# Optimization experiments

Measured on AMD Instinct MI355X. Metric: run time of the kernel, lower is better.

The kernel has to match this reference:

```python
import jax, jax.numpy as jnp
import numpy as np

N = 25000
E = 400000
H = 4        # heads
C = 256      # per-head channels
D_IN = 1024
NEG_SLOPE = 0.2


def setup_inputs() -> dict:
    key = jax.random.key(0)
    k1, k2, k3, k4, k5, k6 = jax.random.split(key, 6)
    x = jax.random.normal(k1, (N, D_IN), dtype=jnp.float32)
    edge_index = jax.random.randint(k2, (2, E), 0, N, dtype=jnp.int64)
    # GATConv parameters
    scale = 1.0 / np.sqrt(D_IN)
    W = jax.random.normal(k3, (D_IN, H * C), dtype=jnp.float32) * scale
    att_src = jax.random.normal(k4, (H, C), dtype=jnp.float32) * 0.1
    att_dst = jax.random.normal(k5, (H, C), dtype=jnp.float32) * 0.1
    bias = jax.random.normal(k6, (H * C,), dtype=jnp.float32) * 0.01
    return {"x": x, "edge_index": edge_index, "W": W,
            "att_src": att_src, "att_dst": att_dst, "bias": bias}


def reference(x, edge_index, W, att_src, att_dst, bias):
    # Dense projection: [N, D_IN] @ [D_IN, H*C] -> [N, H, C]
    xp = (x @ W).reshape(N, H, C)

    # Per-node attention logits [N, H]
    a_src = jnp.einsum('nhc,hc->nh', xp, att_src)
    a_dst = jnp.einsum('nhc,hc->nh', xp, att_dst)

    # PyG default add_self_loops=True
    loops = jnp.arange(N, dtype=edge_index.dtype)
    src = jnp.concatenate([edge_index[0], loops])  # [E+N]
    dst = jnp.concatenate([edge_index[1], loops])  # [E+N]

    # Edge attention logits + LeakyReLU
    e = jax.nn.leaky_relu(a_src[src] + a_dst[dst], NEG_SLOPE)  # [E+N, H]

    # Segment softmax over destination nodes (every node has a self loop)
    m = jax.ops.segment_max(e, dst, num_segments=N)            # [N, H]
    ee = jnp.exp(e - m[dst])
    z = jax.ops.segment_sum(ee, dst, num_segments=N)           # [N, H]
    alpha = ee / z[dst]                                        # [E+N, H]

    # Scatter-weighted aggregation: out[i] = sum_j alpha_ij * xp[j]
    msgs = xp[src] * alpha[:, :, None]                         # [E+N, H, C]
    out = jax.ops.segment_sum(msgs, dst, num_segments=N)       # [N, H, C]

    out = out.reshape(N, H * C) + bias
    # dropout(0.5) is identity in eval mode; act = ReLU
    return jax.nn.relu(out)
```

## Files before the change

### kernel.cpp

```cpp
#include <hip/hip_runtime.h>
#include <hip/hip_bf16.h>
#include <stdint.h>

#define N_NODES 25000
#define M_PAD   25088
#define E_EDGES 400000
#define NE      (E_EDGES + N_NODES)
#define HEADS   4
#define D_DIM   1024
#define NEG_SLOPE 0.2f
#define NBLK_SCAN ((N_NODES + 255) / 256)

using bf16x8  = __attribute__((ext_vector_type(8))) short;
using floatx4 = __attribute__((ext_vector_type(4))) float;
using ushort8 = __attribute__((ext_vector_type(8))) unsigned short;

__device__ __forceinline__ unsigned short f2bf(float f) {
    union { float f; unsigned u; } v{f};
    unsigned r = v.u + 0x7fffu + ((v.u >> 16) & 1u);
    return (unsigned short)(r >> 16);
}
__device__ __forceinline__ float bf2f(unsigned short s) {
    union { unsigned u; float f; } v{(unsigned)s << 16};
    return v.f;
}

__global__ __launch_bounds__(256) void k_convert_x(
        const float* __restrict__ x, unsigned short* __restrict__ xb) {
    int i = blockIdx.x * 256 + threadIdx.x;
    int row = i >> 8;
    if (row >= M_PAD) return;
    ushort4 o;
    if (row < N_NODES) {
        float4 v = ((const float4*)x)[i];
        o = make_ushort4(f2bf(v.x), f2bf(v.y), f2bf(v.z), f2bf(v.w));
    } else {
        o = make_ushort4(0, 0, 0, 0);
    }
    ((ushort4*)xb)[i] = o;
}

__global__ void k_convert_wt(const float* __restrict__ W,
                             unsigned short* __restrict__ Wt) {
    __shared__ float tile[32][33];
    int bx = blockIdx.x, by = blockIdx.y;
    int tx = threadIdx.x, ty = threadIdx.y;
    #pragma unroll
    for (int i = 0; i < 32; i += 8) {
        int k = by * 32 + ty + i;
        int n = bx * 32 + tx;
        tile[ty + i][tx] = W[(size_t)k * D_DIM + n];
    }
    __syncthreads();
    #pragma unroll
    for (int i = 0; i < 32; i += 8) {
        int n = bx * 32 + ty + i;
        int k = by * 32 + tx;
        Wt[(size_t)n * D_DIM + k] = f2bf(tile[tx][ty + i]);
    }
}

__global__ __launch_bounds__(256) void k_gemm(
        const unsigned short* __restrict__ A,
        const unsigned short* __restrict__ Bt,
        unsigned short* __restrict__ C) {
    __shared__ __align__(16) unsigned short As[128 * 32];
    __shared__ __align__(16) unsigned short Bs[128 * 32];

    const int tid  = threadIdx.x;
    const int m0   = blockIdx.x * 128;
    const int n0   = blockIdx.y * 128;
    const int wave = tid >> 6, lane = tid & 63;
    const int wm   = (wave & 1) * 64, wn = (wave >> 1) * 64;
    const int lrow = lane & 15;
    const int quad = lane >> 4;

    const int srow = (lane >> 2);
    const int scol = (lane & 3) * 8;

    floatx4 acc[4][4] = {};

    for (int k0 = 0; k0 < D_DIM; k0 += 32) {
        #pragma unroll
        for (int j = 0; j < 2; ++j) {
            int rbase = wave * 32 + j * 16;
            const unsigned short* ga =
                &A[(size_t)(m0 + rbase + srow) * D_DIM + k0 + scol];
            const unsigned short* gb =
                &Bt[(size_t)(n0 + rbase + srow) * D_DIM + k0 + scol];
            __builtin_amdgcn_global_load_lds(
                (const __attribute__((address_space(1))) void*)ga,
                (__attribute__((address_space(3))) void*)&As[rbase * 32],
                16, 0, 0);
            __builtin_amdgcn_global_load_lds(
                (const __attribute__((address_space(1))) void*)gb,
                (__attribute__((address_space(3))) void*)&Bs[rbase * 32],
                16, 0, 0);
        }
        __syncthreads();

        bf16x8 af[4], bfr[4];
        #pragma unroll
        for (int mi = 0; mi < 4; ++mi)
            af[mi] = *(const bf16x8*)(&As[(wm + mi * 16 + lrow) * 32 + quad * 8]);
        #pragma unroll
        for (int ni = 0; ni < 4; ++ni)
            bfr[ni] = *(const bf16x8*)(&Bs[(wn + ni * 16 + lrow) * 32 + quad * 8]);

        #pragma unroll
        for (int mi = 0; mi < 4; ++mi)
            #pragma unroll
            for (int ni = 0; ni < 4; ++ni)
                acc[mi][ni] = __builtin_amdgcn_mfma_f32_16x16x32_bf16(
                    af[mi], bfr[ni], acc[mi][ni], 0, 0, 0);
        __syncthreads();
    }

    #pragma unroll
    for (int mi = 0; mi < 4; ++mi) {
        #pragma unroll
        for (int ni = 0; ni < 4; ++ni) {
            #pragma unroll
            for (int r = 0; r < 4; ++r) {
                int gm = m0 + wm + mi * 16 + quad * 4 + r;
                int gn = n0 + wn + ni * 16 + lrow;
                C[(size_t)gm * D_DIM + gn] = f2bf(acc[mi][ni][r]);
            }
        }
    }
}

__global__ __launch_bounds__(256) void k_node_logits(
        const unsigned short* __restrict__ xp,
        const float* __restrict__ att_src, const float* __restrict__ att_dst,
        float* __restrict__ a_src, float* __restrict__ a_dst) {
    int n = blockIdx.x;
    int tid = threadIdx.x;
    int h = tid >> 6, lane = tid & 63;
    int c = h * 256 + lane * 4;
    ushort4 v  = *(const ushort4*)(&xp[(size_t)n * D_DIM + c]);
    float4 as  = *(const float4*)(&att_src[c]);
    float4 ad  = *(const float4*)(&att_dst[c]);
    float x0 = bf2f(v.x), x1 = bf2f(v.y), x2 = bf2f(v.z), x3 = bf2f(v.w);
    float s = x0 * as.x + x1 * as.y + x2 * as.z + x3 * as.w;
    float d = x0 * ad.x + x1 * ad.y + x2 * ad.z + x3 * ad.w;
    #pragma unroll
    for (int off = 32; off > 0; off >>= 1) {
        s += __shfl_down(s, off);
        d += __shfl_down(d, off);
    }
    if (lane == 0) { a_src[n * 4 + h] = s; a_dst[n * 4 + h] = d; }
}

__global__ __launch_bounds__(256) void k_deg(
        const int* __restrict__ ei, int* __restrict__ deg) {
    int e = blockIdx.x * 256 + threadIdx.x;
    if (e >= NE) return;
    int d = (e < E_EDGES) ? ei[E_EDGES + e] : (e - E_EDGES);
    atomicAdd(&deg[d], 1);
}

__global__ __launch_bounds__(256) void k_scan1(
        const int* __restrict__ deg, int* __restrict__ rowstart,
        int* __restrict__ blocksum) {
    __shared__ int smem[256];
    int i = blockIdx.x * 256 + threadIdx.x;
    int v = (i < N_NODES) ? deg[i] : 0;
    smem[threadIdx.x] = v;
    __syncthreads();
    #pragma unroll
    for (int off = 1; off < 256; off <<= 1) {
        int t = (threadIdx.x >= off) ? smem[threadIdx.x - off] : 0;
        __syncthreads();
        smem[threadIdx.x] += t;
        __syncthreads();
    }
    if (i < N_NODES) rowstart[i] = smem[threadIdx.x] - v;
    if (threadIdx.x == 255) blocksum[blockIdx.x] = smem[255];
}

__global__ __launch_bounds__(128) void k_scan2(
        const int* __restrict__ blocksum, int* __restrict__ blockoff) {
    __shared__ int smem[128];
    int v = (threadIdx.x < NBLK_SCAN) ? blocksum[threadIdx.x] : 0;
    smem[threadIdx.x] = v;
    __syncthreads();
    #pragma unroll
    for (int off = 1; off < 128; off <<= 1) {
        int t = (threadIdx.x >= off) ? smem[threadIdx.x - off] : 0;
        __syncthreads();
        smem[threadIdx.x] += t;
        __syncthreads();
    }
    blockoff[threadIdx.x] = smem[threadIdx.x] - v;
}

__global__ __launch_bounds__(256) void k_scan3(
        int* __restrict__ rowstart, const int* __restrict__ blockoff) {
    int i = blockIdx.x * 256 + threadIdx.x;
    if (i < N_NODES) rowstart[i] += blockoff[blockIdx.x];
    if (i == 0) rowstart[N_NODES] = NE;
}

__global__ __launch_bounds__(256) void k_edge_exp_scatter(
        const int* __restrict__ ei,
        const float* __restrict__ a_src, const float* __restrict__ a_dst,
        const int* __restrict__ rowstart, int* __restrict__ cursor,
        int* __restrict__ csr_src, float* __restrict__ csr_ee) {
    int e = blockIdx.x * 256 + threadIdx.x;
    if (e >= NE) return;
    int s, d;
    if (e < E_EDGES) { s = ei[e]; d = ei[E_EDGES + e]; }
    else             { s = d = e - E_EDGES; }
    float4 as = *(const float4*)(&a_src[s * 4]);
    float4 ad = *(const float4*)(&a_dst[d * 4]);
    float l0 = as.x + ad.x, l1 = as.y + ad.y, l2 = as.z + ad.z, l3 = as.w + ad.w;
    l0 = l0 > 0.f ? l0 : NEG_SLOPE * l0;
    l1 = l1 > 0.f ? l1 : NEG_SLOPE * l1;
    l2 = l2 > 0.f ? l2 : NEG_SLOPE * l2;
    l3 = l3 > 0.f ? l3 : NEG_SLOPE * l3;
    int pos  = atomicAdd(&cursor[d], 1);
    int slot = rowstart[d] + pos;
    csr_src[slot] = s;
    *(float4*)(&csr_ee[(size_t)slot * 4]) =
        make_float4(__expf(l0), __expf(l1), __expf(l2), __expf(l3));
}

__device__ __forceinline__ void acc8(float* acc, float a, ushort8 v) {
    #pragma unroll
    for (int j = 0; j < 8; ++j) acc[j] += a * bf2f((unsigned short)v[j]);
}

__global__ __launch_bounds__(256) void k_node_aggregate(
        const int* __restrict__ csr_src, const float* __restrict__ csr_ee,
        const int* __restrict__ rowstart,
        const unsigned short* __restrict__ xp,
        const float* __restrict__ bias, float* __restrict__ out) {
    const int tid  = threadIdx.x;
    const int half = tid >> 7;
    const int n    = blockIdx.x * 2 + half;
    const int t    = tid & 127;
    const int row  = rowstart[n];
    const int deg  = rowstart[n + 1] - row;

    __shared__ float zsh[2][4];
    if ((tid & 64) == 0) {
        int lane = tid & 63;
        float z0 = 0.f, z1 = 0.f, z2 = 0.f, z3 = 0.f;
        for (int i = lane; i < deg; i += 64) {
            float4 v = *(const float4*)(&csr_ee[(size_t)(row + i) * 4]);
            z0 += v.x; z1 += v.y; z2 += v.z; z3 += v.w;
        }
        #pragma unroll
        for (int off = 32; off > 0; off >>= 1) {
            z0 += __shfl_down(z0, off);
            z1 += __shfl_down(z1, off);
            z2 += __shfl_down(z2, off);
            z3 += __shfl_down(z3, off);
        }
        if (lane == 0) {
            zsh[half][0] = z0; zsh[half][1] = z1;
            zsh[half][2] = z2; zsh[half][3] = z3;
        }
    }
    __syncthreads();

    const int h = t >> 5;
    const int c = t * 8;
    const float rz = 1.0f / zsh[half][h];

    float acc[8] = {};
    int i = 0;
    for (; i + 4 <= deg; i += 4) {
        int s0 = csr_src[row + i + 0];
        int s1 = csr_src[row + i + 1];
        int s2 = csr_src[row + i + 2];
        int s3 = csr_src[row + i + 3];
        float a0 = csr_ee[(size_t)(row + i + 0) * 4 + h] * rz;
        float a1 = csr_ee[(size_t)(row + i + 1) * 4 + h] * rz;
        float a2 = csr_ee[(size_t)(row + i + 2) * 4 + h] * rz;
        float a3 = csr_ee[(size_t)(row + i + 3) * 4 + h] * rz;
        ushort8 v0 = *(const ushort8*)(&xp[(size_t)s0 * D_DIM + c]);
        ushort8 v1 = *(const ushort8*)(&xp[(size_t)s1 * D_DIM + c]);
        ushort8 v2 = *(const ushort8*)(&xp[(size_t)s2 * D_DIM + c]);
        ushort8 v3 = *(const ushort8*)(&xp[(size_t)s3 * D_DIM + c]);
        acc8(acc, a0, v0);
        acc8(acc, a1, v1);
        acc8(acc, a2, v2);
        acc8(acc, a3, v3);
    }
    for (; i < deg; ++i) {
        int s   = csr_src[row + i];
        float a = csr_ee[(size_t)(row + i) * 4 + h] * rz;
        ushort8 v = *(const ushort8*)(&xp[(size_t)s * D_DIM + c]);
        acc8(acc, a, v);
    }

    float4 b0 = *(const float4*)(&bias[c]);
    float4 b1 = *(const float4*)(&bias[c + 4]);
    float4 o0, o1;
    o0.x = fmaxf(acc[0] + b0.x, 0.f);
    o0.y = fmaxf(acc[1] + b0.y, 0.f);
    o0.z = fmaxf(acc[2] + b0.z, 0.f);
    o0.w = fmaxf(acc[3] + b0.w, 0.f);
    o1.x = fmaxf(acc[4] + b1.x, 0.f);
    o1.y = fmaxf(acc[5] + b1.y, 0.f);
    o1.z = fmaxf(acc[6] + b1.z, 0.f);
    o1.w = fmaxf(acc[7] + b1.w, 0.f);
    *(float4*)(&out[(size_t)n * D_DIM + c])     = o0;
    *(float4*)(&out[(size_t)n * D_DIM + c + 4]) = o1;
}

extern "C" void kernel_launch(void* const* d_in, const int* in_sizes, int n_in,
                              void* d_out, int out_size, void* d_ws, size_t ws_size,
                              hipStream_t stream) {
    const float* x       = (const float*)d_in[0];
    const int*   ei      = (const int*)d_in[1];
    const float* W       = (const float*)d_in[2];
    const float* att_src = (const float*)d_in[3];
    const float* att_dst = (const float*)d_in[4];
    const float* bias    = (const float*)d_in[5];
    float* out = (float*)d_out;

    char* ws = (char*)d_ws;
    size_t off = 0;
    auto alloc = [&](size_t bytes) -> void* {
        void* p = ws + off;
        off = (off + bytes + 255) & ~(size_t)255;
        return p;
    };
    unsigned short* xb   = (unsigned short*)alloc((size_t)M_PAD * D_DIM * 2);
    unsigned short* Wt   = (unsigned short*)alloc((size_t)D_DIM * D_DIM * 2);
    unsigned short* xpb  = (unsigned short*)alloc((size_t)M_PAD * D_DIM * 2);
    float* a_src    = (float*)alloc((size_t)N_NODES * 4 * 4);
    float* a_dst    = (float*)alloc((size_t)N_NODES * 4 * 4);
    int*   deg      = (int*)alloc((size_t)N_NODES * 4);
    int*   rowstart = (int*)alloc((size_t)(N_NODES + 1) * 4);
    int*   cursor   = (int*)alloc((size_t)N_NODES * 4);
    int*   blocksum = (int*)alloc((size_t)NBLK_SCAN * 4);
    int*   blockoff = (int*)alloc((size_t)128 * 4);
    int*   csr_src  = (int*)alloc((size_t)NE * 4);
    float* csr_ee   = (float*)alloc((size_t)NE * 4 * 4);

    hipMemsetAsync(deg, 0, (size_t)N_NODES * 4, stream);
    hipMemsetAsync(cursor, 0, (size_t)N_NODES * 4, stream);

    k_convert_x<<<M_PAD, 256, 0, stream>>>(x, xb);
    k_convert_wt<<<dim3(32, 32), dim3(32, 8), 0, stream>>>(W, Wt);
    k_gemm<<<dim3(M_PAD / 128, D_DIM / 128), 256, 0, stream>>>(xb, Wt, xpb);
    k_node_logits<<<N_NODES, 256, 0, stream>>>(xpb, att_src, att_dst, a_src, a_dst);
    k_deg<<<(NE + 255) / 256, 256, 0, stream>>>(ei, deg);
    k_scan1<<<NBLK_SCAN, 256, 0, stream>>>(deg, rowstart, blocksum);
    k_scan2<<<1, 128, 0, stream>>>(blocksum, blockoff);
    k_scan3<<<NBLK_SCAN, 256, 0, stream>>>(rowstart, blockoff);
    k_edge_exp_scatter<<<(NE + 255) / 256, 256, 0, stream>>>(
        ei, a_src, a_dst, rowstart, cursor, csr_src, csr_ee);
    k_node_aggregate<<<12500, 256, 0, stream>>>(
        csr_src, csr_ee, rowstart, xpb, bias, out);
}
```

Measured before the change: 465.0 us.

## Fuse attention logits into GEMM epilogue and restructure aggregation to one wave per node

The GEMM epilogue now computes per-node attention logits from fp32 accumulators by reducing over 16-lane groups and atomically adding partial sums. This removes the separate node-logits kernel and its re-read of the projected features. The aggregation kernel now gives each node one wave with 16 channels per lane, computing the softmax denominator without shared memory or a block barrier. Several streaming loads and stores are marked nontemporal. The trade-offs are float atomics (order-dependent rounding) and two extra memsets.

```diff
diff --git a/kernel.cpp b/kernel.cpp
--- a/kernel.cpp
+++ b/kernel.cpp
@@ -14,6 +14,7 @@
 using bf16x8  = __attribute__((ext_vector_type(8))) short;
 using floatx4 = __attribute__((ext_vector_type(4))) float;
 using ushort8 = __attribute__((ext_vector_type(8))) unsigned short;
+typedef float  f32x4v __attribute__((ext_vector_type(4)));
 
 __device__ __forceinline__ unsigned short f2bf(float f) {
     union { float f; unsigned u; } v{f};
@@ -32,7 +33,7 @@
     if (row >= M_PAD) return;
     ushort4 o;
     if (row < N_NODES) {
-        float4 v = ((const float4*)x)[i];
+        f32x4v v = __builtin_nontemporal_load((const f32x4v*)x + i);
         o = make_ushort4(f2bf(v.x), f2bf(v.y), f2bf(v.z), f2bf(v.w));
     } else {
         o = make_ushort4(0, 0, 0, 0);
@@ -63,7 +64,9 @@
 __global__ __launch_bounds__(256) void k_gemm(
         const unsigned short* __restrict__ A,
         const unsigned short* __restrict__ Bt,
-        unsigned short* __restrict__ C) {
+        unsigned short* __restrict__ C,
+        const float* __restrict__ att_src, const float* __restrict__ att_dst,
+        float* __restrict__ a_src, float* __restrict__ a_dst) {
     __shared__ __align__(16) unsigned short As[128 * 32];
     __shared__ __align__(16) unsigned short Bs[128 * 32];
 
@@ -128,28 +131,37 @@
             }
         }
     }
-}
-
-__global__ __launch_bounds__(256) void k_node_logits(
-        const unsigned short* __restrict__ xp,
-        const float* __restrict__ att_src, const float* __restrict__ att_dst,
-        float* __restrict__ a_src, float* __restrict__ a_dst) {
-    int n = blockIdx.x;
-    int tid = threadIdx.x;
-    int h = tid >> 6, lane = tid & 63;
-    int c = h * 256 + lane * 4;
-    ushort4 v  = *(const ushort4*)(&xp[(size_t)n * D_DIM + c]);
-    float4 as  = *(const float4*)(&att_src[c]);
-    float4 ad  = *(const float4*)(&att_dst[c]);
-    float x0 = bf2f(v.x), x1 = bf2f(v.y), x2 = bf2f(v.z), x3 = bf2f(v.w);
-    float s = x0 * as.x + x1 * as.y + x2 * as.z + x3 * as.w;
-    float d = x0 * ad.x + x1 * ad.y + x2 * ad.z + x3 * ad.w;
-    #pragma unroll
-    for (int off = 32; off > 0; off >>= 1) {
-        s += __shfl_down(s, off);
-        d += __shfl_down(d, off);
-    }
-    if (lane == 0) { a_src[n * 4 + h] = s; a_dst[n * 4 + h] = d; }
+
+    const int h0 = (n0 + wn) >> 8;
+    float asv[4], adv[4];
+    #pragma unroll
+    for (int ni = 0; ni < 4; ++ni) {
+        int gn = n0 + wn + ni * 16 + lrow;
+        asv[ni] = att_src[gn];
+        adv[ni] = att_dst[gn];
+    }
+    #pragma unroll
+    for (int mi = 0; mi < 4; ++mi) {
+        #pragma unroll
+        for (int r = 0; r < 4; ++r) {
+            float ps = 0.f, pd = 0.f;
+            #pragma unroll
+            for (int ni = 0; ni < 4; ++ni) {
+                ps += acc[mi][ni][r] * asv[ni];
+                pd += acc[mi][ni][r] * adv[ni];
+            }
+            #pragma unroll
+            for (int off = 8; off > 0; off >>= 1) {
+                ps += __shfl_down(ps, off, 16);
+                pd += __shfl_down(pd, off, 16);
+            }
+            if (lrow == 0) {
+                int gm = m0 + wm + mi * 16 + quad * 4 + r;
+                atomicAdd(&a_src[gm * 4 + h0], ps);
+                atomicAdd(&a_dst[gm * 4 + h0], pd);
+            }
+        }
+    }
 }
 
 __global__ __launch_bounds__(256) void k_deg(
@@ -226,9 +238,12 @@
         make_float4(__expf(l0), __expf(l1), __expf(l2), __expf(l3));
 }
 
-__device__ __forceinline__ void acc8(float* acc, float a, ushort8 v) {
-    #pragma unroll
-    for (int j = 0; j < 8; ++j) acc[j] += a * bf2f((unsigned short)v[j]);
+__device__ __forceinline__ void acc16(float* acc, float a,
+                                      ushort8 v0, ushort8 v1) {
+    #pragma unroll
+    for (int j = 0; j < 8; ++j) acc[j]     += a * bf2f((unsigned short)v0[j]);
+    #pragma unroll
+    for (int j = 0; j < 8; ++j) acc[8 + j] += a * bf2f((unsigned short)v1[j]);
 }
 
 __global__ __launch_bounds__(256) void k_node_aggregate(
@@ -237,78 +252,71 @@
         const unsigned short* __restrict__ xp,
         const float* __restrict__ bias, float* __restrict__ out) {
     const int tid  = threadIdx.x;
-    const int half = tid >> 7;
-    const int n    = blockIdx.x * 2 + half;
-    const int t    = tid & 127;
+    const int lane = tid & 63;
+    const int n    = blockIdx.x * 4 + (tid >> 6);
     const int row  = rowstart[n];
     const int deg  = rowstart[n + 1] - row;
 
-    __shared__ float zsh[2][4];
-    if ((tid & 64) == 0) {
-        int lane = tid & 63;
-        float z0 = 0.f, z1 = 0.f, z2 = 0.f, z3 = 0.f;
-        for (int i = lane; i < deg; i += 64) {
-            float4 v = *(const float4*)(&csr_ee[(size_t)(row + i) * 4]);
-            z0 += v.x; z1 += v.y; z2 += v.z; z3 += v.w;
-        }
-        #pragma unroll
-        for (int off = 32; off > 0; off >>= 1) {
-            z0 += __shfl_down(z0, off);
-            z1 += __shfl_down(z1, off);
-            z2 += __shfl_down(z2, off);
-            z3 += __shfl_down(z3, off);
-        }
-        if (lane == 0) {
-            zsh[half][0] = z0; zsh[half][1] = z1;
-            zsh[half][2] = z2; zsh[half][3] = z3;
-        }
-    }
-    __syncthreads();
-
-    const int h = t >> 5;
-    const int c = t * 8;
-    const float rz = 1.0f / zsh[half][h];
-
-    float acc[8] = {};
+    float z0 = 0.f, z1 = 0.f, z2 = 0.f, z3 = 0.f;
+    for (int i = lane; i < deg; i += 64) {
+        f32x4v v = __builtin_nontemporal_load((const f32x4v*)csr_ee + (row + i));
+        z0 += v.x; z1 += v.y; z2 += v.z; z3 += v.w;
+    }
+    #pragma unroll
+    for (int off = 32; off > 0; off >>= 1) {
+        z0 += __shfl_xor(z0, off);
+        z1 += __shfl_xor(z1, off);
+        z2 += __shfl_xor(z2, off);
+        z3 += __shfl_xor(z3, off);
+    }
+    const int h = lane >> 4;
+    float zh = (h == 0) ? z0 : (h == 1) ? z1 : (h == 2) ? z2 : z3;
+    const float rz = 1.0f / zh;
+
+    const int c = h * 256 + (lane & 15) * 16;
+
+    float acc[16] = {};
     int i = 0;
     for (; i + 4 <= deg; i += 4) {
-        int s0 = csr_src[row + i + 0];
-        int s1 = csr_src[row + i + 1];
-        int s2 = csr_src[row + i + 2];
-        int s3 = csr_src[row + i + 3];
-        float a0 = csr_ee[(size_t)(row + i + 0) * 4 + h] * rz;
-        float a1 = csr_ee[(size_t)(row + i + 1) * 4 + h] * rz;
-        float a2 = csr_ee[(size_t)(row + i + 2) * 4 + h] * rz;
-        float a3 = csr_ee[(size_t)(row + i + 3) * 4 + h] * rz;
-        ushort8 v0 = *(const ushort8*)(&xp[(size_t)s0 * D_DIM + c]);
-        ushort8 v1 = *(const ushort8*)(&xp[(size_t)s1 * D_DIM + c]);
-        ushort8 v2 = *(const ushort8*)(&xp[(size_t)s2 * D_DIM + c]);
-        ushort8 v3 = *(const ushort8*)(&xp[(size_t)s3 * D_DIM + c]);
-        acc8(acc, a0, v0);
-        acc8(acc, a1, v1);
-        acc8(acc, a2, v2);
-        acc8(acc, a3, v3);
+        int s0 = __builtin_nontemporal_load(&csr_src[row + i + 0]);
+        int s1 = __builtin_nontemporal_load(&csr_src[row + i + 1]);
+        int s2 = __builtin_nontemporal_load(&csr_src[row + i + 2]);
+        int s3 = __builtin_nontemporal_load(&csr_src[row + i + 3]);
+        float a0 = __builtin_nontemporal_load(&csr_ee[(size_t)(row+i+0)*4+h]) * rz;
+        float a1 = __builtin_nontemporal_load(&csr_ee[(size_t)(row+i+1)*4+h]) * rz;
+        float a2 = __builtin_nontemporal_load(&csr_ee[(size_t)(row+i+2)*4+h]) * rz;
+        float a3 = __builtin_nontemporal_load(&csr_ee[(size_t)(row+i+3)*4+h]) * rz;
+        ushort8 v00 = *(const ushort8*)(&xp[(size_t)s0 * D_DIM + c]);
+        ushort8 v01 = *(const ushort8*)(&xp[(size_t)s0 * D_DIM + c + 8]);
+        ushort8 v10 = *(const ushort8*)(&xp[(size_t)s1 * D_DIM + c]);
+        ushort8 v11 = *(const ushort8*)(&xp[(size_t)s1 * D_DIM + c + 8]);
+        ushort8 v20 = *(const ushort8*)(&xp[(size_t)s2 * D_DIM + c]);
+        ushort8 v21 = *(const ushort8*)(&xp[(size_t)s2 * D_DIM + c + 8]);
+        ushort8 v30 = *(const ushort8*)(&xp[(size_t)s3 * D_DIM + c]);
+        ushort8 v31 = *(const ushort8*)(&xp[(size_t)s3 * D_DIM + c + 8]);
+        acc16(acc, a0, v00, v01);
+        acc16(acc, a1, v10, v11);
+        acc16(acc, a2, v20, v21);
+        acc16(acc, a3, v30, v31);
     }
     for (; i < deg; ++i) {
-        int s   = csr_src[row + i];
-        float a = csr_ee[(size_t)(row + i) * 4 + h] * rz;
-        ushort8 v = *(const ushort8*)(&xp[(size_t)s * D_DIM + c]);
-        acc8(acc, a, v);
-    }
-
-    float4 b0 = *(const float4*)(&bias[c]);
-    float4 b1 = *(const float4*)(&bias[c + 4]);
-    float4 o0, o1;
-    o0.x = fmaxf(acc[0] + b0.x, 0.f);
-    o0.y = fmaxf(acc[1] + b0.y, 0.f);
-    o0.z = fmaxf(acc[2] + b0.z, 0.f);
-    o0.w = fmaxf(acc[3] + b0.w, 0.f);
-    o1.x = fmaxf(acc[4] + b1.x, 0.f);
-    o1.y = fmaxf(acc[5] + b1.y, 0.f);
-    o1.z = fmaxf(acc[6] + b1.z, 0.f);
-    o1.w = fmaxf(acc[7] + b1.w, 0.f);
-    *(float4*)(&out[(size_t)n * D_DIM + c])     = o0;
-    *(float4*)(&out[(size_t)n * D_DIM + c + 4]) = o1;
+        int s   = __builtin_nontemporal_load(&csr_src[row + i]);
+        float a = __builtin_nontemporal_load(&csr_ee[(size_t)(row+i)*4+h]) * rz;
+        ushort8 v0 = *(const ushort8*)(&xp[(size_t)s * D_DIM + c]);
+        ushort8 v1 = *(const ushort8*)(&xp[(size_t)s * D_DIM + c + 8]);
+        acc16(acc, a, v0, v1);
+    }
+
+    #pragma unroll
+    for (int q = 0; q < 4; ++q) {
+        float4 b = *(const float4*)(&bias[c + q * 4]);
+        f32x4v o;
+        o.x = fmaxf(acc[q * 4 + 0] + b.x, 0.f);
+        o.y = fmaxf(acc[q * 4 + 1] + b.y, 0.f);
+        o.z = fmaxf(acc[q * 4 + 2] + b.z, 0.f);
+        o.w = fmaxf(acc[q * 4 + 3] + b.w, 0.f);
+        __builtin_nontemporal_store(o, (f32x4v*)&out[(size_t)n * D_DIM + c + q * 4]);
+    }
 }
 
 extern "C" void kernel_launch(void* const* d_in, const int* in_sizes, int n_in,
@@ -332,8 +340,8 @@
     unsigned short* xb   = (unsigned short*)alloc((size_t)M_PAD * D_DIM * 2);
     unsigned short* Wt   = (unsigned short*)alloc((size_t)D_DIM * D_DIM * 2);
     unsigned short* xpb  = (unsigned short*)alloc((size_t)M_PAD * D_DIM * 2);
-    float* a_src    = (float*)alloc((size_t)N_NODES * 4 * 4);
-    float* a_dst    = (float*)alloc((size_t)N_NODES * 4 * 4);
+    float* a_src    = (float*)alloc((size_t)M_PAD * 4 * 4);
+    float* a_dst    = (float*)alloc((size_t)M_PAD * 4 * 4);
     int*   deg      = (int*)alloc((size_t)N_NODES * 4);
     int*   rowstart = (int*)alloc((size_t)(N_NODES + 1) * 4);
     int*   cursor   = (int*)alloc((size_t)N_NODES * 4);
@@ -344,17 +352,19 @@
 
     hipMemsetAsync(deg, 0, (size_t)N_NODES * 4, stream);
     hipMemsetAsync(cursor, 0, (size_t)N_NODES * 4, stream);
+    hipMemsetAsync(a_src, 0, (size_t)M_PAD * 4 * 4, stream);
+    hipMemsetAsync(a_dst, 0, (size_t)M_PAD * 4 * 4, stream);
 
     k_convert_x<<<M_PAD, 256, 0, stream>>>(x, xb);
     k_convert_wt<<<dim3(32, 32), dim3(32, 8), 0, stream>>>(W, Wt);
-    k_gemm<<<dim3(M_PAD / 128, D_DIM / 128), 256, 0, stream>>>(xb, Wt, xpb);
-    k_node_logits<<<N_NODES, 256, 0, stream>>>(xpb, att_src, att_dst, a_src, a_dst);
+    k_gemm<<<dim3(M_PAD / 128, D_DIM / 128), 256, 0, stream>>>(
+        xb, Wt, xpb, att_src, att_dst, a_src, a_dst);
     k_deg<<<(NE + 255) / 256, 256, 0, stream>>>(ei, deg);
     k_scan1<<<NBLK_SCAN, 256, 0, stream>>>(deg, rowstart, blocksum);
     k_scan2<<<1, 128, 0, stream>>>(blocksum, blockoff);
     k_scan3<<<NBLK_SCAN, 256, 0, stream>>>(rowstart, blockoff);
     k_edge_exp_scatter<<<(NE + 255) / 256, 256, 0, stream>>>(
         ei, a_src, a_dst, rowstart, cursor, csr_src, csr_ee);
-    k_node_aggregate<<<12500, 256, 0, stream>>>(
+    k_node_aggregate<<<6250, 256, 0, stream>>>(
         csr_src, csr_ee, rowstart, xpb, bias, out);
 }
```

Result: slower. 517.5 us (+11.3%).
